# Performance work log

Hardware: AMD Instinct MI355X
Metric: run time of the kernel (lower is better)

## Reference

```python
import jax, jax.numpy as jnp
import numpy as np

B = 65536
OBS_DIM = 1129      # 37 self + 39 * 28 other-agent features
N_OTHERS = 39
N_ATT = 40          # agent_num * 2 == 1 + N_OTHERS
EM = 32
HID = 32
N_ACT = 21


def setup_inputs() -> dict:
    key = jax.random.key(0)
    ks = jax.random.split(key, 8)
    s = 0.1  # weight init scale
    return {
        "obs": jax.random.normal(ks[0], (B, OBS_DIM), dtype=jnp.float32),
        "W_al": jax.random.normal(ks[1], (OBS_DIM, N_ATT), dtype=jnp.float32) * s,
        "b_al": jnp.zeros((N_ATT,), dtype=jnp.float32),
        "W_self": jax.random.normal(ks[2], (37, EM), dtype=jnp.float32) * s,
        "b_self": jnp.zeros((EM,), dtype=jnp.float32),
        "W_other": jax.random.normal(ks[3], (28, EM), dtype=jnp.float32) * s,
        "b_other": jnp.zeros((EM,), dtype=jnp.float32),
        "W_attout": jax.random.normal(ks[4], (EM, HID), dtype=jnp.float32) * s,
        "b_attout": jnp.zeros((HID,), dtype=jnp.float32),
        "W_emb": jax.random.normal(ks[5], (HID, HID), dtype=jnp.float32) * s,
        "b_emb": jnp.zeros((HID,), dtype=jnp.float32),
        "W_out": jax.random.normal(ks[6], (HID, N_ACT), dtype=jnp.float32) * s,
        "b_out": jnp.zeros((N_ACT,), dtype=jnp.float32),
    }


def reference(obs, W_al, b_al, W_self, b_self, W_other, b_other,
              W_attout, b_attout, W_emb, b_emb, W_out, b_out):
    # attention weights over the (self + others) encodings; torch f.softmax
    # default on 2D is dim=1
    att_w = jax.nn.softmax(obs @ W_al + b_al, axis=1)            # [B, 40]
    # per-agent encodings (self encoding has NO relu in the original)
    self_enc = obs[:, :37] @ W_self + b_self                     # [B, em]
    others = obs[:, 37:].reshape(obs.shape[0], N_OTHERS, 28)     # [B, 39, 28]
    other_enc = jax.nn.relu(jnp.einsum('bnd,de->bne', others, W_other) + b_other)
    enc = jnp.concatenate([self_enc[:, None, :], other_enc], axis=1)  # [B, 40, em]
    # bmm(att_w[:,None,:], enc).squeeze(1)
    att_out = jnp.einsum('ba,bae->be', att_w, enc)               # [B, em]
    h = jax.nn.relu(att_out @ W_attout + b_attout)               # get_attention_layer out
    h = jax.nn.relu(h @ W_emb + b_emb)                           # embedding_layer
    return h @ W_out + b_out                                     # out_layer -> Q values
```

## Files before the change

kernel.cpp:

```cpp
#include <hip/hip_runtime.h>


typedef __bf16 bf16x8 __attribute__((ext_vector_type(8)));
typedef float  f32x4  __attribute__((ext_vector_type(4)));

constexpr int OBS = 1129;

#define MFMA(a, b, c) __builtin_amdgcn_mfma_f32_16x16x32_bf16((a), (b), (c), 0, 0, 0)

__device__ __forceinline__ float4 ld4(const float* p) {
    float4 v;
    __builtin_memcpy(&v, p, 16);
    return v;
}

__device__ __forceinline__ void split8(const float* a, bf16x8& h, bf16x8& l) {
#pragma unroll
    for (int i = 0; i < 8; ++i) {
        __bf16 hb = (__bf16)a[i];
        h[i] = hb;
        l[i] = (__bf16)(a[i] - (float)hb);
    }
}

__device__ __forceinline__ f32x4 mm3(bf16x8 ah, bf16x8 al, bf16x8 bh, bf16x8 bl, f32x4 c) {
    c = MFMA(ah, bh, c);
    c = MFMA(ah, bl, c);
    c = MFMA(al, bh, c);
    return c;
}

__device__ __forceinline__ void glds16(const void* g, void* l) {
    __builtin_amdgcn_global_load_lds((const __attribute__((address_space(1))) void*)g,
                                     (__attribute__((address_space(3))) void*)l, 16, 0, 0);
}

__global__ void prep_weights(const float* __restrict__ W_al,
                             const float* __restrict__ W_self,
                             const float* __restrict__ W_oth,
                             const float* __restrict__ W_ao,
                             const float* __restrict__ W_emb,
                             const float* __restrict__ W_out,
                             bf16x8* __restrict__ ws)
{
    const int u = blockIdx.x;
    const int l = threadIdx.x;
    const int s = l >> 4, col = l & 15;
    const float* W; int K, N, ld, c, t, shift = 0;
    if (u < 108)      { c = u / 3;         t = u % 3;         W = W_al;   K = 1129; N = 40; ld = 40; }
    else if (u < 112) { c = (u - 108) / 2; t = (u - 108) & 1; W = W_self; K = 37;   N = 32; ld = 32; }
    else if (u < 114) { c = 0;             t = u - 112;       W = W_oth;  K = 28;   N = 32; ld = 32; shift = 1; }
    else if (u < 116) { c = 0;             t = u - 114;       W = W_ao;   K = 32;   N = 32; ld = 32; }
    else if (u < 118) { c = 0;             t = u - 116;       W = W_emb;  K = 32;   N = 32; ld = 32; }
    else              { c = 0;             t = u - 118;       W = W_out;  K = 32;   N = 21; ld = 21; }
    const int j = t * 16 + col;
    bf16x8 h, lo;
#pragma unroll
    for (int i = 0; i < 8; ++i) {
        int k = c * 32 + s * 8 + i;
        int kk = k - shift;
        float w = (kk >= 0 && kk < K && j < N) ? W[kk * ld + j] : 0.f;
        __bf16 hb = (__bf16)w;
        h[i]  = hb;
        lo[i] = (__bf16)(w - (float)hb);
    }
    ws[u * 128 + l]      = h;
    ws[u * 128 + 64 + l] = lo;
}

__global__ __launch_bounds__(256, 2)
void qnet_fwd(const float* __restrict__ obs,
              const float* __restrict__ b_al,
              const float* __restrict__ b_ao,
              const float* __restrict__ b_emb,
              const float* __restrict__ b_out,
              const bf16x8* __restrict__ wf,
              float* __restrict__ out)
{
    __shared__ __align__(16) char arena[49152];
    __shared__ float sW[4 * 656];

    const int t    = threadIdx.x;
    const int lane = t & 63;
    const int wv   = t >> 6;
    const int s    = lane >> 4;
    const int cq   = lane & 15;
    const int rowbase = blockIdx.x * 64 + wv * 16;
    const float* __restrict__ orow = obs + (size_t)(rowbase + cq) * OBS;
    const char* __restrict__ wfb = (const char*)wf;
    float* __restrict__ sWw = sW + wv * 656;

    const f32x4 zf = {0.f, 0.f, 0.f, 0.f};

    const size_t aB0 = (size_t)(rowbase + (lane >> 3)) * OBS + 4 * ((lane & 7) ^ (lane >> 3));
    const size_t aB1 = aB0 + (size_t)8 * OBS;
    const unsigned rdA0 = (unsigned)(cq * 128 + (((2 * s)     ^ (cq & 7)) << 4));
    const unsigned rdA1 = (unsigned)(cq * 128 + (((2 * s + 1) ^ (cq & 7)) << 4));

    char* const Abase = arena + wv * 2048;
    char* const Bbase = arena + 32768;
    const int bt = wv % 3;

#define STAGE_A(K, C)                                                             \
    do {                                                                          \
        char* _d = Abase + (K) * 8192;                                            \
        glds16(obs + aB0 + (C) * 32, _d);                                         \
        glds16(obs + aB1 + (C) * 32, _d + 1024);                                  \
    } while (0)
#define STAGE_BH(K, C)                                                            \
    do {                                                                          \
        glds16(wfb + (size_t)(C) * 6144 + (size_t)bt * 2048 + lane * 16,          \
               Bbase + (K) * 3072 + bt * 1024);                                   \
    } while (0)

    f32x4 acc0 = zf, acc1 = zf, acc2 = zf;

#define P1_MATH(FA0, FA1, BP)                                                     \
    do {                                                                          \
        float _av[8] = {(FA0).x, (FA0).y, (FA0).z, (FA0).w,                       \
                        (FA1).x, (FA1).y, (FA1).z, (FA1).w};                      \
        bf16x8 _ah, _al; split8(_av, _ah, _al);                                   \
        const char* _bp = (const char*)(BP);                                      \
        bf16x8 b0 = *(const bf16x8*)(_bp + lane * 16);                            \
        bf16x8 b1 = *(const bf16x8*)(_bp + 1024 + lane * 16);                     \
        bf16x8 b2 = *(const bf16x8*)(_bp + 2048 + lane * 16);                     \
        __builtin_amdgcn_s_setprio(1);                                            \
        acc0 = MFMA(_ah, b0, acc0); acc0 = MFMA(_al, b0, acc0);                   \
        acc1 = MFMA(_ah, b1, acc1); acc1 = MFMA(_al, b1, acc1);                   \
        acc2 = MFMA(_ah, b2, acc2); acc2 = MFMA(_al, b2, acc2);                   \
        __builtin_amdgcn_s_setprio(0);                                            \
    } while (0)

    STAGE_A(0, 0); STAGE_BH(0, 0);
    STAGE_A(1, 1); STAGE_BH(1, 1);
    STAGE_A(2, 2); STAGE_BH(2, 2);

    for (int c = 0; c < 32; ++c) {
        const int kc = c & 3, kn = (c + 3) & 3;
        asm volatile("s_waitcnt vmcnt(6)" ::: "memory");
        __builtin_amdgcn_s_barrier();
        __builtin_amdgcn_sched_barrier(0);
        const char* ab = Abase + kc * 8192;
        float4 fa0 = *(const float4*)(ab + rdA0);
        float4 fa1 = *(const float4*)(ab + rdA1);
        asm volatile("s_waitcnt lgkmcnt(0)" ::: "memory");
        __builtin_amdgcn_sched_barrier(0);
        STAGE_A(kn, c + 3);
        STAGE_BH(kn, c + 3);
        P1_MATH(fa0, fa1, Bbase + kc * 3072);
    }
    {
        asm volatile("s_waitcnt vmcnt(6)" ::: "memory");
        __builtin_amdgcn_s_barrier();
        __builtin_amdgcn_sched_barrier(0);
        const char* ab = Abase + 0 * 8192;
        float4 fa0 = *(const float4*)(ab + rdA0);
        float4 fa1 = *(const float4*)(ab + rdA1);
        asm volatile("s_waitcnt lgkmcnt(0)" ::: "memory");
        __builtin_amdgcn_sched_barrier(0);
        STAGE_BH(3, 35);
        P1_MATH(fa0, fa1, Bbase + 0 * 3072);
    }
    {
        asm volatile("s_waitcnt vmcnt(4)" ::: "memory");
        __builtin_amdgcn_s_barrier();
        __builtin_amdgcn_sched_barrier(0);
        const char* ab = Abase + 1 * 8192;
        float4 fa0 = *(const float4*)(ab + rdA0);
        float4 fa1 = *(const float4*)(ab + rdA1);
        P1_MATH(fa0, fa1, Bbase + 1 * 3072);
    }
    {
        asm volatile("s_waitcnt vmcnt(1)" ::: "memory");
        __builtin_amdgcn_s_barrier();
        __builtin_amdgcn_sched_barrier(0);
        const char* ab = Abase + 2 * 8192;
        float4 fa0 = *(const float4*)(ab + rdA0);
        float4 fa1 = *(const float4*)(ab + rdA1);
        P1_MATH(fa0, fa1, Bbase + 2 * 3072);
    }
    {
        asm volatile("s_waitcnt vmcnt(0)" ::: "memory");
        __builtin_amdgcn_s_barrier();
        __builtin_amdgcn_sched_barrier(0);
        float av[8] = {0, 0, 0, 0, 0, 0, 0, 0};
        if (s == 0) {
            float4 p = ld4(orow + 1120), q = ld4(orow + 1124);
            av[0] = p.x; av[1] = p.y; av[2] = p.z; av[3] = p.w;
            av[4] = q.x; av[5] = q.y; av[6] = q.z; av[7] = q.w;
        } else if (s == 1) {
            av[0] = orow[1128];
        }
        float4 fa0 = {av[0], av[1], av[2], av[3]};
        float4 fa1 = {av[4], av[5], av[6], av[7]};
        P1_MATH(fa0, fa1, Bbase + 3 * 3072);
    }
    __syncthreads();

    {
        const float bal0 = b_al[cq];
        const float bal1 = b_al[16 + cq];
        const bool  v2m  = (cq < 8);
        const float bal2 = v2m ? b_al[32 + cq] : 0.f;
#pragma unroll
        for (int j = 0; j < 4; ++j) {
            float v0 = acc0[j] + bal0, v1 = acc1[j] + bal1, vv = acc2[j] + bal2;
            float m = fmaxf(fmaxf(v0, v1), v2m ? vv : -3.4e38f);
#pragma unroll
            for (int d = 1; d < 16; d <<= 1) m = fmaxf(m, __shfl_xor(m, d));
            float e0 = __expf(v0 - m), e1 = __expf(v1 - m);
            float e2 = v2m ? __expf(vv - m) : 0.f;
            float sm = e0 + e1 + e2;
#pragma unroll
            for (int d = 1; d < 16; d <<= 1) sm += __shfl_xor(sm, d);
            float inv = 1.f / sm;
            const int row = s * 4 + j;
            sWw[row * 41 + cq]      = e0 * inv;
            sWw[row * 41 + 16 + cq] = e1 * inv;
            if (v2m) sWw[row * 41 + 32 + cq] = e2 * inv;
        }
    }

    const bf16x8* bo = wf + (size_t)112 * 128;
    const bf16x8 Boh0 = bo[lane],       Bol0 = bo[64 + lane];
    const bf16x8 Boh1 = bo[128 + lane], Bol1 = bo[192 + lane];

    f32x4 at0 = zf, at1 = zf;
    {
        f32x4 e0 = zf, e1 = zf;
        {
            float4 p = ld4(orow + s * 8), q = ld4(orow + s * 8 + 4);
            float av[8] = {p.x, p.y, p.z, p.w, q.x, q.y, q.z, q.w};
            bf16x8 ah, al; split8(av, ah, al);
            const bf16x8* bu = wf + (size_t)108 * 128;
            e0 = mm3(ah, al, bu[lane],       bu[64 + lane],  e0);
            e1 = mm3(ah, al, bu[128 + lane], bu[192 + lane], e1);
        }
        {
            float av[8] = {0, 0, 0, 0, 0, 0, 0, 0};
            if (s == 0) {
                float4 p = ld4(orow + 32);
                av[0] = p.x; av[1] = p.y; av[2] = p.z; av[3] = p.w;
                av[4] = orow[36];
            }
            bf16x8 ah, al; split8(av, ah, al);
            const bf16x8* bu = wf + (size_t)110 * 128;
            e0 = mm3(ah, al, bu[lane],       bu[64 + lane],  e0);
            e1 = mm3(ah, al, bu[128 + lane], bu[192 + lane], e1);
        }
#pragma unroll
        for (int j = 0; j < 4; ++j) {
            float w0 = sWw[(s * 4 + j) * 41];
            at0[j] = w0 * e0[j];
            at1[j] = w0 * e1[j];
        }
    }

    asm volatile("s_waitcnt vmcnt(0)" ::: "memory");

    const unsigned uE = (unsigned)((lane & 15) ^ (lane >> 4));
    const unsigned uO = (unsigned)((lane & 15) ^ (4 + (lane >> 4)));
    const size_t pE = (size_t)(rowbase +     (lane >> 4)) * OBS + 36 + 4 * uE;
    const size_t pO = (size_t)(rowbase + 4 + (lane >> 4)) * OBS + 36 + 4 * uO;
    const size_t p8 = (size_t)8 * OBS;

    char* const Pbase = arena + wv * 12288;

#define STAGE_P(K, W)                                                             \
    do {                                                                          \
        char* _d = Pbase + (K) * 4096;                                            \
        glds16(obs + pE + 56 * (W),      _d);                                     \
        glds16(obs + pO + 56 * (W),      _d + 1024);                              \
        glds16(obs + pE + p8 + 56 * (W), _d + 2048);                              \
        glds16(obs + pO + p8 + 56 * (W), _d + 3072);                              \
    } while (0)

    const unsigned rdP00 = rdA0;
    (void)rdP00;
    const unsigned rdQ00 = (unsigned)(cq * 256 + (((2 * s)     ^ (cq & 7)) << 4));
    const unsigned rdQ01 = (unsigned)(cq * 256 + (((2 * s + 1) ^ (cq & 7)) << 4));
    const unsigned rdQ10 = (unsigned)(cq * 256 + (((7 + 2 * s) ^ (cq & 7)) << 4));
    const unsigned rdQ11 = (unsigned)(cq * 256 + (((8 + 2 * s) ^ (cq & 7)) << 4));

#define PROC2(N, U0, U1)                                                          \
    do {                                                                          \
        bf16x8 _ah;                                                               \
        _ah[0] = (__bf16)(U0).x; _ah[1] = (__bf16)(U0).y;                         \
        _ah[2] = (__bf16)(U0).z; _ah[3] = (__bf16)(U0).w;                         \
        _ah[4] = (__bf16)(U1).x; _ah[5] = (__bf16)(U1).y;                         \
        _ah[6] = (__bf16)(U1).z; _ah[7] = (__bf16)(U1).w;                         \
        f32x4 _e0 = MFMA(_ah, Boh0, zf); _e0 = MFMA(_ah, Bol0, _e0);              \
        f32x4 _e1 = MFMA(_ah, Boh1, zf); _e1 = MFMA(_ah, Bol1, _e1);              \
        _Pragma("unroll")                                                         \
        for (int _j = 0; _j < 4; ++_j) {                                          \
            float _wn = sWw[(s * 4 + _j) * 41 + 1 + (N)];                         \
            at0[_j] += _wn * fmaxf(_e0[_j], 0.f);                                 \
            at1[_j] += _wn * fmaxf(_e1[_j], 0.f);                                 \
        }                                                                         \
    } while (0)

#define P2_READS(K)                                                               \
    const char* _q = Pbase + (K) * 4096;                                          \
    float4 u00 = *(const float4*)(_q + rdQ00);                                    \
    float4 u01 = *(const float4*)(_q + rdQ01);                                    \
    float4 u10 = *(const float4*)(_q + rdQ10);                                    \
    float4 u11 = *(const float4*)(_q + rdQ11)

    STAGE_P(0, 0);
    STAGE_P(1, 1);
    STAGE_P(2, 2);

    for (int w = 0; w < 16; ++w) {
        const int kc = w % 3, kn = (w + 3) % 3;
        asm volatile("s_waitcnt vmcnt(8)" ::: "memory");
        __builtin_amdgcn_sched_barrier(0);
        P2_READS(kc);
        asm volatile("s_waitcnt lgkmcnt(0)" ::: "memory");
        __builtin_amdgcn_sched_barrier(0);
        STAGE_P(kn, w + 3);
        __builtin_amdgcn_s_setprio(1);
        PROC2(2 * w,     u00, u01);
        PROC2(2 * w + 1, u10, u11);
        __builtin_amdgcn_s_setprio(0);
    }
    {
        asm volatile("s_waitcnt vmcnt(8)" ::: "memory");
        __builtin_amdgcn_sched_barrier(0);
        P2_READS(1);
        PROC2(32, u00, u01);
        PROC2(33, u10, u11);
    }
    {
        asm volatile("s_waitcnt vmcnt(4)" ::: "memory");
        __builtin_amdgcn_sched_barrier(0);
        P2_READS(2);
        PROC2(34, u00, u01);
        PROC2(35, u10, u11);
    }
    {
        asm volatile("s_waitcnt vmcnt(0)" ::: "memory");
        __builtin_amdgcn_sched_barrier(0);
        P2_READS(0);
        PROC2(36, u00, u01);
        PROC2(37, u10, u11);
    }
    {
        const float* op = orow + 1100;
        float av[8];
        if (s < 3) {
            float4 p = ld4(op + s * 8), q = ld4(op + s * 8 + 4);
            av[0] = p.x; av[1] = p.y; av[2] = p.z; av[3] = p.w;
            av[4] = q.x; av[5] = q.y; av[6] = q.z; av[7] = q.w;
        } else {
            float4 p = ld4(op + 24);
            av[0] = p.x; av[1] = p.y; av[2] = p.z; av[3] = p.w;
            av[4] = op[28];
            av[5] = 0.f; av[6] = 0.f; av[7] = 0.f;
        }
        float4 u0 = {av[0], av[1], av[2], av[3]};
        float4 u1 = {av[4], av[5], av[6], av[7]};
        PROC2(38, u0, u1);
    }

    __bf16* hiw = (__bf16*)Pbase;
    __bf16* low = hiw + 640;
    f32x4 x0 = at0, x1 = at1;
#pragma unroll
    for (int L = 0; L < 3; ++L) {
        const int unit = 114 + L * 2;
        const float* bias = (L == 0) ? b_ao : (L == 1) ? b_emb : b_out;
        const int N = (L == 2) ? 21 : 32;
#pragma unroll
        for (int j = 0; j < 4; ++j) {
            const int row = s * 4 + j;
            __bf16 h0 = (__bf16)x0[j];
            hiw[row * 40 + cq] = h0;
            low[row * 40 + cq] = (__bf16)(x0[j] - (float)h0);
            __bf16 h1 = (__bf16)x1[j];
            hiw[row * 40 + 16 + cq] = h1;
            low[row * 40 + 16 + cq] = (__bf16)(x1[j] - (float)h1);
        }
        bf16x8 ah = *(const bf16x8*)&hiw[cq * 40 + s * 8];
        bf16x8 al = *(const bf16x8*)&low[cq * 40 + s * 8];
        const bf16x8* bu = wf + (size_t)unit * 128;
        f32x4 y0 = mm3(ah, al, bu[lane],       bu[64 + lane],  zf);
        f32x4 y1 = mm3(ah, al, bu[128 + lane], bu[192 + lane], zf);
        const float bc0 = bias[cq];
        const float bc1 = (16 + cq < N) ? bias[16 + cq] : 0.f;
#pragma unroll
        for (int j = 0; j < 4; ++j) {
            y0[j] += bc0;
            y1[j] += bc1;
            if (L < 2) { y0[j] = fmaxf(y0[j], 0.f); y1[j] = fmaxf(y1[j], 0.f); }
        }
        x0 = y0; x1 = y1;
    }

#pragma unroll
    for (int j = 0; j < 4; ++j) {
        const int row = rowbase + s * 4 + j;
        out[(size_t)row * 21 + cq] = x0[j];
        if (cq < 5) out[(size_t)row * 21 + 16 + cq] = x1[j];
    }
}

extern "C" void kernel_launch(void* const* d_in, const int* in_sizes, int n_in,
                              void* d_out, int out_size, void* d_ws, size_t ws_size,
                              hipStream_t stream) {
    const float* obs    = (const float*)d_in[0];
    const float* W_al   = (const float*)d_in[1];
    const float* b_al   = (const float*)d_in[2];
    const float* W_self = (const float*)d_in[3];
    const float* W_oth  = (const float*)d_in[5];
    const float* W_ao   = (const float*)d_in[7];
    const float* b_ao   = (const float*)d_in[8];
    const float* W_emb  = (const float*)d_in[9];
    const float* b_emb  = (const float*)d_in[10];
    const float* W_out  = (const float*)d_in[11];
    const float* b_out  = (const float*)d_in[12];
    float* out = (float*)d_out;
    bf16x8* ws = (bf16x8*)d_ws;

    prep_weights<<<120, 64, 0, stream>>>(W_al, W_self, W_oth, W_ao, W_emb, W_out, ws);

    const int B = in_sizes[0] / OBS;
    qnet_fwd<<<B / 64, 256, 0, stream>>>(obs, b_al, b_ao, b_emb, b_out,
                                         (const bf16x8*)ws, out);
}
```

Before: 108.3 us.

## Keep softmax weights in registers via shuffles and shrink LDS for three blocks/CU

Removes the per-wave shared-memory softmax weight table and instead keeps the attention weights in the MFMA accumulator registers, fetching each agent's weight with a lane shuffle. The phase-1 A staging ring is cut from four to three slots so the arena shrinks, and launch bounds are raised to request three blocks per CU. This trades LDS traffic and footprint for extra cross-lane shuffles and register pressure. The shallower A prefetch ring may expose more load latency.

```diff
diff --git a/kernel.cpp b/kernel.cpp
--- a/kernel.cpp
+++ b/kernel.cpp
@@ -68,7 +68,7 @@
     ws[u * 128 + 64 + l] = lo;
 }
 
-__global__ __launch_bounds__(256, 2)
+__global__ __launch_bounds__(256, 3)
 void qnet_fwd(const float* __restrict__ obs,
               const float* __restrict__ b_al,
               const float* __restrict__ b_ao,
@@ -78,17 +78,16 @@
               float* __restrict__ out)
 {
     __shared__ __align__(16) char arena[49152];
-    __shared__ float sW[4 * 656];
 
     const int t    = threadIdx.x;
     const int lane = t & 63;
     const int wv   = t >> 6;
     const int s    = lane >> 4;
     const int cq   = lane & 15;
+    const int grp  = lane & 48;
     const int rowbase = blockIdx.x * 64 + wv * 16;
     const float* __restrict__ orow = obs + (size_t)(rowbase + cq) * OBS;
     const char* __restrict__ wfb = (const char*)wf;
-    float* __restrict__ sWw = sW + wv * 656;
 
     const f32x4 zf = {0.f, 0.f, 0.f, 0.f};
 
@@ -98,7 +97,7 @@
     const unsigned rdA1 = (unsigned)(cq * 128 + (((2 * s + 1) ^ (cq & 7)) << 4));
 
     char* const Abase = arena + wv * 2048;
-    char* const Bbase = arena + 32768;
+    char* const Bbase = arena + 24576;
     const int bt = wv % 3;
 
 #define STAGE_A(K, C)                                                             \
@@ -136,48 +135,48 @@
     STAGE_A(2, 2); STAGE_BH(2, 2);
 
     for (int c = 0; c < 32; ++c) {
-        const int kc = c & 3, kn = (c + 3) & 3;
+        const int k3 = c % 3, kb = c & 3, kbn = (c + 3) & 3;
         asm volatile("s_waitcnt vmcnt(6)" ::: "memory");
         __builtin_amdgcn_s_barrier();
         __builtin_amdgcn_sched_barrier(0);
-        const char* ab = Abase + kc * 8192;
+        const char* ab = Abase + k3 * 8192;
         float4 fa0 = *(const float4*)(ab + rdA0);
         float4 fa1 = *(const float4*)(ab + rdA1);
         asm volatile("s_waitcnt lgkmcnt(0)" ::: "memory");
         __builtin_amdgcn_sched_barrier(0);
-        STAGE_A(kn, c + 3);
-        STAGE_BH(kn, c + 3);
-        P1_MATH(fa0, fa1, Bbase + kc * 3072);
+        STAGE_A(k3, c + 3);
+        STAGE_BH(kbn, c + 3);
+        P1_MATH(fa0, fa1, Bbase + kb * 3072);
     }
     {
         asm volatile("s_waitcnt vmcnt(6)" ::: "memory");
         __builtin_amdgcn_s_barrier();
         __builtin_amdgcn_sched_barrier(0);
-        const char* ab = Abase + 0 * 8192;
+        const char* ab = Abase + (32 % 3) * 8192;
         float4 fa0 = *(const float4*)(ab + rdA0);
         float4 fa1 = *(const float4*)(ab + rdA1);
         asm volatile("s_waitcnt lgkmcnt(0)" ::: "memory");
         __builtin_amdgcn_sched_barrier(0);
         STAGE_BH(3, 35);
-        P1_MATH(fa0, fa1, Bbase + 0 * 3072);
+        P1_MATH(fa0, fa1, Bbase + (32 & 3) * 3072);
     }
     {
         asm volatile("s_waitcnt vmcnt(4)" ::: "memory");
         __builtin_amdgcn_s_barrier();
         __builtin_amdgcn_sched_barrier(0);
-        const char* ab = Abase + 1 * 8192;
+        const char* ab = Abase + (33 % 3) * 8192;
         float4 fa0 = *(const float4*)(ab + rdA0);
         float4 fa1 = *(const float4*)(ab + rdA1);
-        P1_MATH(fa0, fa1, Bbase + 1 * 3072);
+        P1_MATH(fa0, fa1, Bbase + (33 & 3) * 3072);
     }
     {
         asm volatile("s_waitcnt vmcnt(1)" ::: "memory");
         __builtin_amdgcn_s_barrier();
         __builtin_amdgcn_sched_barrier(0);
-        const char* ab = Abase + 2 * 8192;
+        const char* ab = Abase + (34 % 3) * 8192;
         float4 fa0 = *(const float4*)(ab + rdA0);
         float4 fa1 = *(const float4*)(ab + rdA1);
-        P1_MATH(fa0, fa1, Bbase + 2 * 3072);
+        P1_MATH(fa0, fa1, Bbase + (34 & 3) * 3072);
     }
     {
         asm volatile("s_waitcnt vmcnt(0)" ::: "memory");
@@ -214,10 +213,9 @@
 #pragma unroll
             for (int d = 1; d < 16; d <<= 1) sm += __shfl_xor(sm, d);
             float inv = 1.f / sm;
-            const int row = s * 4 + j;
-            sWw[row * 41 + cq]      = e0 * inv;
-            sWw[row * 41 + 16 + cq] = e1 * inv;
-            if (v2m) sWw[row * 41 + 32 + cq] = e2 * inv;
+            acc0[j] = e0 * inv;
+            acc1[j] = e1 * inv;
+            acc2[j] = v2m ? e2 * inv : 0.f;
         }
     }
 
@@ -250,7 +248,7 @@
         }
 #pragma unroll
         for (int j = 0; j < 4; ++j) {
-            float w0 = sWw[(s * 4 + j) * 41];
+            float w0 = __shfl(acc0[j], grp);
             at0[j] = w0 * e0[j];
             at1[j] = w0 * e1[j];
         }
@@ -275,14 +273,12 @@
         glds16(obs + pO + p8 + 56 * (W), _d + 3072);                              \
     } while (0)
 
-    const unsigned rdP00 = rdA0;
-    (void)rdP00;
     const unsigned rdQ00 = (unsigned)(cq * 256 + (((2 * s)     ^ (cq & 7)) << 4));
     const unsigned rdQ01 = (unsigned)(cq * 256 + (((2 * s + 1) ^ (cq & 7)) << 4));
     const unsigned rdQ10 = (unsigned)(cq * 256 + (((7 + 2 * s) ^ (cq & 7)) << 4));
     const unsigned rdQ11 = (unsigned)(cq * 256 + (((8 + 2 * s) ^ (cq & 7)) << 4));
 
-#define PROC2(N, U0, U1)                                                          \
+#define PROC2(N, U0, U1, WC)                                                      \
     do {                                                                          \
         bf16x8 _ah;                                                               \
         _ah[0] = (__bf16)(U0).x; _ah[1] = (__bf16)(U0).y;                         \
@@ -291,9 +287,10 @@
         _ah[6] = (__bf16)(U1).z; _ah[7] = (__bf16)(U1).w;                         \
         f32x4 _e0 = MFMA(_ah, Boh0, zf); _e0 = MFMA(_ah, Bol0, _e0);              \
         f32x4 _e1 = MFMA(_ah, Boh1, zf); _e1 = MFMA(_ah, Bol1, _e1);              \
+        const int _src = grp | (((N) + 1) & 15);                                  \
         _Pragma("unroll")                                                         \
         for (int _j = 0; _j < 4; ++_j) {                                          \
-            float _wn = sWw[(s * 4 + _j) * 41 + 1 + (N)];                         \
+            float _wn = __shfl((WC)[_j], _src);                                   \
             at0[_j] += _wn * fmaxf(_e0[_j], 0.f);                                 \
             at1[_j] += _wn * fmaxf(_e1[_j], 0.f);                                 \
         }                                                                         \
@@ -306,43 +303,50 @@
     float4 u10 = *(const float4*)(_q + rdQ10);                                    \
     float4 u11 = *(const float4*)(_q + rdQ11)
 
+#define P2_ITER(W, VM, DOSTAGE, WC0, WC1)                                         \
+    do {                                                                          \
+        asm volatile("s_waitcnt vmcnt(" #VM ")" ::: "memory");                    \
+        __builtin_amdgcn_sched_barrier(0);                                        \
+        P2_READS((W) % 3);                                                        \
+        asm volatile("s_waitcnt lgkmcnt(0)" ::: "memory");                        \
+        __builtin_amdgcn_sched_barrier(0);                                        \
+        if (DOSTAGE) STAGE_P((W) % 3, (W) + 3);                                   \
+        __builtin_amdgcn_s_setprio(1);                                            \
+        PROC2(2 * (W),     u00, u01, WC0);                                        \
+        PROC2(2 * (W) + 1, u10, u11, WC1);                                        \
+        __builtin_amdgcn_s_setprio(0);                                            \
+    } while (0)
+
     STAGE_P(0, 0);
     STAGE_P(1, 1);
     STAGE_P(2, 2);
 
-    for (int w = 0; w < 16; ++w) {
-        const int kc = w % 3, kn = (w + 3) % 3;
+    for (int w = 0; w < 7; ++w)
+        P2_ITER(w, 8, true, acc0, acc0);
+    P2_ITER(7, 8, true, acc0, acc1);
+    for (int w = 8; w < 15; ++w)
+        P2_ITER(w, 8, true, acc1, acc1);
+    P2_ITER(15, 8, true, acc1, acc2);
+    {
         asm volatile("s_waitcnt vmcnt(8)" ::: "memory");
         __builtin_amdgcn_sched_barrier(0);
-        P2_READS(kc);
-        asm volatile("s_waitcnt lgkmcnt(0)" ::: "memory");
-        __builtin_amdgcn_sched_barrier(0);
-        STAGE_P(kn, w + 3);
-        __builtin_amdgcn_s_setprio(1);
-        PROC2(2 * w,     u00, u01);
-        PROC2(2 * w + 1, u10, u11);
-        __builtin_amdgcn_s_setprio(0);
-    }
-    {
-        asm volatile("s_waitcnt vmcnt(8)" ::: "memory");
-        __builtin_amdgcn_sched_barrier(0);
         P2_READS(1);
-        PROC2(32, u00, u01);
-        PROC2(33, u10, u11);
+        PROC2(32, u00, u01, acc2);
+        PROC2(33, u10, u11, acc2);
     }
     {
         asm volatile("s_waitcnt vmcnt(4)" ::: "memory");
         __builtin_amdgcn_sched_barrier(0);
         P2_READS(2);
-        PROC2(34, u00, u01);
-        PROC2(35, u10, u11);
+        PROC2(34, u00, u01, acc2);
+        PROC2(35, u10, u11, acc2);
     }
     {
         asm volatile("s_waitcnt vmcnt(0)" ::: "memory");
         __builtin_amdgcn_sched_barrier(0);
         P2_READS(0);
-        PROC2(36, u00, u01);
-        PROC2(37, u10, u11);
+        PROC2(36, u00, u01, acc2);
+        PROC2(37, u10, u11, acc2);
     }
     {
         const float* op = orow + 1100;
@@ -359,7 +363,7 @@
         }
         float4 u0 = {av[0], av[1], av[2], av[3]};
         float4 u1 = {av[4], av[5], av[6], av[7]};
-        PROC2(38, u0, u1);
+        PROC2(38, u0, u1, acc2);
     }
 
     __bf16* hiw = (__bf16*)Pbase;
```

Measured after the change: 339.8 us. +213.7%, slower.
